# Performance work log

Measured on AMD Instinct MI355X. Metric: run time of the kernel, lower is better.

Reference implementation:

```python
import jax, jax.numpy as jnp
import numpy as np

# YOLOv2 anchors (grid units), 5 anchors, anchor_step=2
ANCHORS = np.array([[1.3221, 1.73145], [3.19275, 4.00944], [5.05587, 8.09892],
                    [9.47112, 4.84053], [11.2364, 10.0071]], dtype=np.float32)
NUM_CLASSES = 2
NOOBJECT_SCALE = 1.0
OBJECT_SCALE = 5.0
COORD_SCALE = 1.0
CLASS_SCALE = 1.0
SIL_THRESH = 0.6
T = 50  # max targets per image


def iou_cwh(b1, b2):
    # boxes (..., 4) as (cx, cy, w, h); broadcasting IoU, faithful to bbox_iou(x1y1x2y2=False)
    x1, y1, w1, h1 = b1[..., 0], b1[..., 1], b1[..., 2], b1[..., 3]
    x2, y2, w2, h2 = b2[..., 0], b2[..., 1], b2[..., 2], b2[..., 3]
    uw = jnp.maximum(x1 + w1 * 0.5, x2 + w2 * 0.5) - jnp.minimum(x1 - w1 * 0.5, x2 - w2 * 0.5)
    uh = jnp.maximum(y1 + h1 * 0.5, y2 + h2 * 0.5) - jnp.minimum(y1 - h1 * 0.5, y2 - h2 * 0.5)
    cw = w1 + w2 - uw
    ch = h1 + h2 - uh
    carea = jnp.where((cw <= 0) | (ch <= 0), 0.0, cw * ch)
    return carea / (w1 * h1 + w2 * h2 - carea)


def yolo_v2_loss(output, target):
    anchors = jnp.asarray(ANCHORS)
    nA, nC = anchors.shape[0], NUM_CLASSES
    nB, _, nH, nW = output.shape
    out5 = output.reshape(nB, nA, 5 + nC + 1, nH, nW)
    aw, ah = anchors[:, 0], anchors[:, 1]

    # ---------- detached predicted boxes (torch used .data) ----------
    po = jax.lax.stop_gradient(out5)
    gx_grid = jnp.arange(nW, dtype=output.dtype)
    gy_grid = jnp.arange(nH, dtype=output.dtype)
    px = jax.nn.sigmoid(po[:, :, 0]) + gx_grid[None, None, None, :]
    py = jax.nn.sigmoid(po[:, :, 1]) + gy_grid[None, None, :, None]
    pw = jnp.exp(po[:, :, 2]) * aw[None, :, None, None]
    ph = jnp.exp(po[:, :, 3]) * ah[None, :, None, None]
    pred = jnp.stack([px, py, pw, ph], -1).reshape(nB, nA * nH * nW, 4)  # (nB, nP, 4)

    # ---------- parse targets ----------
    tgt = target.reshape(nB, T, 6)  # (cls, x, y, w, h, lr)
    tcls_v = tgt[..., 0]
    gx = tgt[..., 1] * nW
    gy = tgt[..., 2] * nH
    gw = tgt[..., 3] * nW
    gh = tgt[..., 4] * nH
    lr_v = tgt[..., 5]
    # torch breaks at first x==0; emulate with cumulative validity
    valid = jnp.cumprod((tgt[..., 1] != 0).astype(jnp.int32), axis=1).astype(bool)

    # ---------- silence mask: max IoU of every pred box vs all gt ----------
    gt = jnp.stack([gx, gy, gw, gh], -1)  # (nB, T, 4)
    ious = iou_cwh(pred[:, :, None, :], gt[:, None, :, :])  # (nB, nP, T)
    cur_ious = jnp.where(valid[:, None, :], ious, 0.0).max(-1)  # (nB, nP)
    conf_mask0 = jnp.where(cur_ious > SIL_THRESH, 0.0, NOOBJECT_SCALE).reshape(-1)

    # ---------- best anchor per gt (centered IoU, argmax == first strict max) ----------
    z = jnp.zeros_like(gw)
    gt0 = jnp.stack([z, z, gw, gh], -1)[:, :, None, :]  # (nB, T, 1, 4)
    za = jnp.zeros_like(aw)
    an0 = jnp.stack([za, za, aw, ah], -1)[None, None, :, :]  # (1, 1, nA, 4)
    best_n = jnp.argmax(iou_cwh(an0, gt0), axis=-1)  # (nB, T)

    gi = gx.astype(jnp.int32)
    gj = gy.astype(jnp.int32)
    aw_b = aw[best_n]
    ah_b = ah[best_n]
    tx_v = gx - gi
    ty_v = gy - gj
    tw_v = jnp.log(gw / aw_b)
    th_v = jnp.log(gh / ah_b)
    idx_in_b = best_n * (nH * nW) + gj * nW + gi  # (nB, T)
    pred_at = jnp.take_along_axis(pred, idx_in_b[:, :, None], axis=1)  # (nB, T, 4)
    tconf_v = iou_cwh(gt, pred_at)  # (nB, T)

    Ntot = nB * nA * nH * nW
    flat_idx = jnp.where(valid, jnp.arange(nB)[:, None] * (nA * nH * nW) + idx_in_b, Ntot)
    one = jnp.ones_like(tx_v)
    # rows: coord_mask, cls_mask, conf_mask, tx, ty, tw, th, tconf, tcls, lr_mask, tconf_lr
    vals = jnp.stack([one, one, OBJECT_SCALE * one, tx_v, ty_v, tw_v, th_v,
                      tconf_v, tcls_v, one, lr_v], 0)  # (11, nB, T)
    state0 = jnp.zeros((11, Ntot), output.dtype).at[2].set(conf_mask0)

    def body(st, inp):
        i, v = inp
        return st.at[:, i].set(v, mode='drop'), None

    state, _ = jax.lax.scan(body, state0, (flat_idx.T, jnp.transpose(vals, (2, 0, 1))))
    state = jax.lax.stop_gradient(state)
    shp = (nB, nA, nH, nW)
    (coord_mask, cls_mask, conf_mask, tx, ty, tw, th,
     tconf, tcls, lr_mask, tconf_lr) = [state[i].reshape(shp) for i in range(11)]

    # ---------- differentiable predictions ----------
    x = jax.nn.sigmoid(out5[:, :, 0])
    y = jax.nn.sigmoid(out5[:, :, 1])
    w = out5[:, :, 2]
    h = out5[:, :, 3]
    conf = jax.nn.sigmoid(out5[:, :, 4])
    conf_lr = jax.nn.sigmoid(out5[:, :, 5 + nC])
    # torch: view(nB*nA, nC, nH*nW).transpose(1,2) -> row order (b, a, h, w)
    cls_logits = jnp.transpose(out5[:, :, 5:5 + nC], (0, 1, 3, 4, 2)).reshape(-1, nC)

    def mse_half(a, b, m):
        return 0.5 * jnp.sum((a * m - b * m) ** 2)

    loss_x = COORD_SCALE * mse_half(x, tx, coord_mask)
    loss_y = COORD_SCALE * mse_half(y, ty, coord_mask)
    loss_w = COORD_SCALE * mse_half(w, tw, coord_mask)
    loss_h = COORD_SCALE * mse_half(h, th, coord_mask)
    loss_conf = mse_half(conf, tconf, jnp.sqrt(conf_mask))
    logp = jax.nn.log_softmax(cls_logits, axis=-1)
    tcls_flat = tcls.reshape(-1).astype(jnp.int32)
    ce = -jnp.take_along_axis(logp, tcls_flat[:, None], axis=1)[:, 0]
    loss_cls = CLASS_SCALE * jnp.sum(ce * cls_mask.reshape(-1))
    loss_conf_lr = mse_half(conf_lr, tconf_lr, lr_mask)
    loss = loss_x + loss_y + loss_w + loss_h + loss_conf + loss_cls + 0.5 * loss_conf_lr
    return loss / nB


def setup_inputs() -> dict:
    key = jax.random.key(0)
    k1, k2, k3, k4, k5 = jax.random.split(key, 5)
    nB, nH, nW = 16, 96, 96
    nA, nC = 5, 2
    output = jax.random.normal(k1, (nB, nA * (5 + nC + 1), nH, nW), jnp.float32) * 0.5
    # targets: (cls, x, y, w, h, lr) per slot, all 50 slots valid (x != 0)
    cls = jax.random.randint(k2, (nB, T, 1), 0, nC).astype(jnp.float32)
    xy = jax.random.uniform(k3, (nB, T, 2), minval=0.05, maxval=0.95)
    wh = jax.random.uniform(k4, (nB, T, 2), minval=0.05, maxval=0.5)
    lr = jax.random.uniform(k5, (nB, T, 1))
    target = jnp.concatenate([cls, xy, wh, lr], axis=-1).reshape(nB, T * 6)
    return {"output": output, "target": target}


def reference(output, target):
    return yolo_v2_loss(output, target)
```

## Files before the change

kernel.cpp:

```cpp
#include <hip/hip_runtime.h>
#include <math.h>

#define NB 16
#define NA 5
#define NH 96
#define NW 96
#define TT 50
#define HW (NH*NW)
#define APB (NA*HW)
#define CPT 4

__device__ __constant__ float c_aw[NA] = {1.3221f, 3.19275f, 5.05587f, 9.47112f, 11.2364f};
__device__ __constant__ float c_ah[NA] = {1.73145f, 4.00944f, 8.09892f, 4.84053f, 10.0071f};

__device__ __forceinline__ float sigmoidf(float x) { return 1.0f / (1.0f + __expf(-x)); }

__global__ void prep_kernel(const float* __restrict__ target,
                            const float* __restrict__ outp,
                            float* __restrict__ gt,
                            float* __restrict__ out) {
    int b = blockIdx.x;
    int t = threadIdx.x;
    __shared__ float s_gxl[TT], s_gxr[TT], s_gyl[TT], s_gyr[TT], s_g06n[TT];
    __shared__ int   s_cell[TT], s_valid[TT];

    float xraw = (t < TT) ? target[(b*TT + t)*6 + 1] : 1.0f;
    unsigned long long m = __ballot(xraw != 0.0f);

    int valid = 0, best = 0, cell = -1, gi = 0, gj = 0;
    float gx=0, gy=0, gw=1, gh=1, tcls=0, lr=0;
    float gxl=0, gxr=0, gyl=0, gyr=0, g06n=-1e30f;
    if (t < TT) {
        valid = (((~m) & ((2ull << t) - 1ull)) == 0ull) ? 1 : 0;
        const float* tg = target + (b*TT + t)*6;
        tcls = tg[0];
        gx = tg[1]*NW; gy = tg[2]*NH; gw = tg[3]*NW; gh = tg[4]*NH;
        lr = tg[5];
        float bestiou = -1.0f;
        for (int a = 0; a < NA; ++a) {
            float inter = fminf(gw, c_aw[a]) * fminf(gh, c_ah[a]);
            float iou = inter / (gw*gh + c_aw[a]*c_ah[a] - inter);
            if (iou > bestiou) { bestiou = iou; best = a; }
        }
        gi = (int)gx; gj = (int)gy;
        cell = best*HW + gj*NW + gi;
        if (valid) {
            gxl = gx - 0.5f*gw; gxr = gx + 0.5f*gw;
            gyl = gy - 0.5f*gh; gyr = gy + 0.5f*gh;
            g06n = -0.6f*gw*gh;
        }
        s_gxl[t] = gxl; s_gxr[t] = gxr; s_gyl[t] = gyl; s_gyr[t] = gyr;
        s_g06n[t] = g06n;
        s_cell[t] = valid ? cell : -1;
        s_valid[t] = valid;
        float* r = gt + (b*TT + t)*8;
        r[0] = gxl; r[1] = gxr; r[2] = gyl; r[3] = gyr; r[4] = g06n;
        r[5] = 0.0f; r[6] = 0.0f; r[7] = 0.0f;
    }
    __syncthreads();

    float acc = 0.0f;
    if (t < TT && valid) {
        int winner = 1;
        for (int u = t + 1; u < TT; ++u)
            if (s_valid[u] && s_cell[u] == cell) { winner = 0; break; }
        if (winner) {
            int a = cell / HW;
            int rem = cell - a*HW;
            const float* base = outp + (size_t)((b*NA + a)*8)*HW + rem;
            float o0 = base[0*HW], o1 = base[1*HW], o2 = base[2*HW], o3 = base[3*HW];
            float o4 = base[4*HW], o5 = base[5*HW], o6 = base[6*HW], o7 = base[7*HW];
            float sx = sigmoidf(o0), sy = sigmoidf(o1);
            float px = sx + (float)gi, py = sy + (float)gj;
            float pw = __expf(o2) * c_aw[a];
            float ph = __expf(o3) * c_ah[a];
            float pxl = px - 0.5f*pw, pxr = px + 0.5f*pw;
            float pyl = py - 0.5f*ph, pyr = py + 0.5f*ph;
            float parea = pw*ph, p6 = 0.6f*parea;
            float maxv = -1e30f;
            for (int u = 0; u < TT; ++u) {
                float cw = fminf(pxr, s_gxr[u]) - fmaxf(pxl, s_gxl[u]);
                float ch = fminf(pyr, s_gyr[u]) - fmaxf(pyl, s_gyl[u]);
                float carea = fmaxf(cw, 0.0f) * fmaxf(ch, 0.0f);
                maxv = fmaxf(maxv, fmaf(1.6f, carea, s_g06n[u]));
            }
            float conf = sigmoidf(o4);
            float noobj = (maxv > p6) ? 0.0f : 0.5f*conf*conf;
            float cw = fminf(pxr, gxr) - fmaxf(pxl, gxl);
            float ch = fminf(pyr, gyr) - fmaxf(pyl, gyl);
            float carea = fmaxf(cw, 0.0f) * fmaxf(ch, 0.0f);
            float tconf = carea / (parea + gw*gh - carea);
            float dc = conf - tconf;
            acc = 2.5f*dc*dc;
            float tx = gx - (float)gi, ty = gy - (float)gj;
            float tw = logf(gw / c_aw[best]), th = logf(gh / c_ah[best]);
            float dx = sx - tx, dy = sy - ty, dw = o2 - tw, dh = o3 - th;
            acc += 0.5f*(dx*dx + dy*dy + dw*dw + dh*dh);
            float mm  = fmaxf(o5, o6);
            float lse = mm + __logf(__expf(o5 - mm) + __expf(o6 - mm));
            acc += lse - ((tcls != 0.0f) ? o6 : o5);
            float dl = sigmoidf(o7) - lr;
            acc += 0.25f*dl*dl;
            acc -= noobj;
        }
    }
    for (int off = 32; off > 0; off >>= 1) acc += __shfl_down(acc, off, 64);
    if (t == 0) atomicAdd(out, acc * (1.0f/NB));
}

__global__ __launch_bounds__(256)
void loss_kernel(const float* __restrict__ outp,
                 const float* __restrict__ gt,
                 float* __restrict__ loss) {
    int b   = blockIdx.y;
    int tid = threadIdx.x;
    int q     = blockIdx.x*256 + tid;
    int cell0 = q*CPT;
    int a   = cell0 / HW;
    int rem = cell0 - a*HW;
    int j   = rem / NW;
    int i0  = rem - j*NW;

    const float* base = outp + (size_t)((b*NA + a)*8)*HW + rem;
    float4 v0 = *(const float4*)(base + 0*HW);
    float4 v1 = *(const float4*)(base + 1*HW);
    float4 v2 = *(const float4*)(base + 2*HW);
    float4 v3 = *(const float4*)(base + 3*HW);
    float4 v4 = *(const float4*)(base + 4*HW);
    float o0[CPT] = {v0.x, v0.y, v0.z, v0.w};
    float o1[CPT] = {v1.x, v1.y, v1.z, v1.w};
    float o2[CPT] = {v2.x, v2.y, v2.z, v2.w};
    float o3[CPT] = {v3.x, v3.y, v3.z, v3.w};
    float o4[CPT] = {v4.x, v4.y, v4.z, v4.w};

    float aw = c_aw[a], ah = c_ah[a];
    float pxl[CPT], pxr[CPT], pyl[CPT], pyr[CPT], p6[CPT], maxv[CPT];
    #pragma unroll
    for (int c = 0; c < CPT; ++c) {
        float sx = sigmoidf(o0[c]), sy = sigmoidf(o1[c]);
        float px = sx + (float)(i0 + c);
        float py = sy + (float)j;
        float pw = __expf(o2[c]) * aw;
        float ph = __expf(o3[c]) * ah;
        pxl[c] = px - 0.5f*pw; pxr[c] = px + 0.5f*pw;
        pyl[c] = py - 0.5f*ph; pyr[c] = py + 0.5f*ph;
        p6[c]  = 0.6f*(pw*ph);
        maxv[c] = -1e30f;
    }

    const float* g = gt + b*(TT*8);
    #pragma unroll 2
    for (int t = 0; t < TT; ++t) {
        const float* r = g + t*8;
        float gxl = r[0], gxr = r[1], gyl = r[2], gyr = r[3], g06n = r[4];
        #pragma unroll
        for (int c = 0; c < CPT; ++c) {
            float cw = fminf(pxr[c], gxr) - fmaxf(pxl[c], gxl);
            float ch = fminf(pyr[c], gyr) - fmaxf(pyl[c], gyl);
            float carea = fmaxf(cw, 0.0f) * fmaxf(ch, 0.0f);
            maxv[c] = fmaxf(maxv[c], fmaf(1.6f, carea, g06n));
        }
    }

    float acc = 0.0f;
    #pragma unroll
    for (int c = 0; c < CPT; ++c) {
        float conf = sigmoidf(o4[c]);
        acc += (maxv[c] > p6[c]) ? 0.0f : 0.5f*conf*conf;
    }

    for (int off = 32; off > 0; off >>= 1) acc += __shfl_down(acc, off, 64);
    __shared__ float ssum[4];
    int lane = tid & 63, wid = tid >> 6;
    if (lane == 0) ssum[wid] = acc;
    __syncthreads();
    if (tid == 0) {
        float s = (ssum[0] + ssum[1]) + (ssum[2] + ssum[3]);
        atomicAdd(loss, s * (1.0f/NB));
    }
}

extern "C" void kernel_launch(void* const* d_in, const int* in_sizes, int n_in,
                              void* d_out, int out_size, void* d_ws, size_t ws_size,
                              hipStream_t stream) {
    const float* output = (const float*)d_in[0];
    const float* target = (const float*)d_in[1];
    float* gtbuf = (float*)d_ws;
    float* out   = (float*)d_out;

    hipMemsetAsync(out, 0, (size_t)out_size*sizeof(float), stream);
    hipLaunchKernelGGL(prep_kernel, dim3(NB), dim3(64), 0, stream,
                       target, output, gtbuf, out);
    dim3 grid(APB/(256*CPT), NB);
    hipLaunchKernelGGL(loss_kernel, grid, dim3(256), 0, stream,
                       output, gtbuf, out);
}
```

Measured before the change: 97.88 us.

## Move per-target object loss into main loss kernel via cell-to-target map

The prep kernel no longer computes object-cell losses. It writes ground-truth box data, per-target coefficients and a dense cell-to-target index map, which is cleared with a memset of 0xFF. The main kernel loads the box table into shared memory and, for each cell, either computes the full object loss or the no-object term. This removes the serial per-target work and the per-target global box re-reads. It adds a 2.9MB memset and an int4 map read per thread.

```diff
diff --git a/kernel.cpp b/kernel.cpp
--- a/kernel.cpp
+++ b/kernel.cpp
@@ -16,20 +16,18 @@
 __device__ __forceinline__ float sigmoidf(float x) { return 1.0f / (1.0f + __expf(-x)); }
 
 __global__ void prep_kernel(const float* __restrict__ target,
-                            const float* __restrict__ outp,
-                            float* __restrict__ gt,
-                            float* __restrict__ out) {
+                            float* __restrict__ gth,
+                            float* __restrict__ gtc,
+                            int* __restrict__ map) {
     int b = blockIdx.x;
     int t = threadIdx.x;
-    __shared__ float s_gxl[TT], s_gxr[TT], s_gyl[TT], s_gyr[TT], s_g06n[TT];
-    __shared__ int   s_cell[TT], s_valid[TT];
+    __shared__ int s_cell[TT], s_valid[TT];
 
     float xraw = (t < TT) ? target[(b*TT + t)*6 + 1] : 1.0f;
     unsigned long long m = __ballot(xraw != 0.0f);
 
     int valid = 0, best = 0, cell = -1, gi = 0, gj = 0;
     float gx=0, gy=0, gw=1, gh=1, tcls=0, lr=0;
-    float gxl=0, gxr=0, gyl=0, gyr=0, g06n=-1e30f;
     if (t < TT) {
         valid = (((~m) & ((2ull << t) - 1ull)) == 0ull) ? 1 : 0;
         const float* tg = target + (b*TT + t)*6;
@@ -44,76 +42,48 @@
         }
         gi = (int)gx; gj = (int)gy;
         cell = best*HW + gj*NW + gi;
-        if (valid) {
-            gxl = gx - 0.5f*gw; gxr = gx + 0.5f*gw;
-            gyl = gy - 0.5f*gh; gyr = gy + 0.5f*gh;
-            g06n = -0.6f*gw*gh;
-        }
-        s_gxl[t] = gxl; s_gxr[t] = gxr; s_gyl[t] = gyl; s_gyr[t] = gyr;
-        s_g06n[t] = g06n;
-        s_cell[t] = valid ? cell : -1;
+        s_cell[t]  = valid ? cell : -1;
         s_valid[t] = valid;
-        float* r = gt + (b*TT + t)*8;
-        r[0] = gxl; r[1] = gxr; r[2] = gyl; r[3] = gyr; r[4] = g06n;
-        r[5] = 0.0f; r[6] = 0.0f; r[7] = 0.0f;
     }
     __syncthreads();
-
-    float acc = 0.0f;
-    if (t < TT && valid) {
-        int winner = 1;
-        for (int u = t + 1; u < TT; ++u)
-            if (s_valid[u] && s_cell[u] == cell) { winner = 0; break; }
-        if (winner) {
-            int a = cell / HW;
-            int rem = cell - a*HW;
-            const float* base = outp + (size_t)((b*NA + a)*8)*HW + rem;
-            float o0 = base[0*HW], o1 = base[1*HW], o2 = base[2*HW], o3 = base[3*HW];
-            float o4 = base[4*HW], o5 = base[5*HW], o6 = base[6*HW], o7 = base[7*HW];
-            float sx = sigmoidf(o0), sy = sigmoidf(o1);
-            float px = sx + (float)gi, py = sy + (float)gj;
-            float pw = __expf(o2) * c_aw[a];
-            float ph = __expf(o3) * c_ah[a];
-            float pxl = px - 0.5f*pw, pxr = px + 0.5f*pw;
-            float pyl = py - 0.5f*ph, pyr = py + 0.5f*ph;
-            float parea = pw*ph, p6 = 0.6f*parea;
-            float maxv = -1e30f;
-            for (int u = 0; u < TT; ++u) {
-                float cw = fminf(pxr, s_gxr[u]) - fmaxf(pxl, s_gxl[u]);
-                float ch = fminf(pyr, s_gyr[u]) - fmaxf(pyl, s_gyl[u]);
-                float carea = fmaxf(cw, 0.0f) * fmaxf(ch, 0.0f);
-                maxv = fmaxf(maxv, fmaf(1.6f, carea, s_g06n[u]));
-            }
-            float conf = sigmoidf(o4);
-            float noobj = (maxv > p6) ? 0.0f : 0.5f*conf*conf;
-            float cw = fminf(pxr, gxr) - fmaxf(pxl, gxl);
-            float ch = fminf(pyr, gyr) - fmaxf(pyl, gyl);
-            float carea = fmaxf(cw, 0.0f) * fmaxf(ch, 0.0f);
-            float tconf = carea / (parea + gw*gh - carea);
-            float dc = conf - tconf;
-            acc = 2.5f*dc*dc;
-            float tx = gx - (float)gi, ty = gy - (float)gj;
-            float tw = logf(gw / c_aw[best]), th = logf(gh / c_ah[best]);
-            float dx = sx - tx, dy = sy - ty, dw = o2 - tw, dh = o3 - th;
-            acc += 0.5f*(dx*dx + dy*dy + dw*dw + dh*dh);
-            float mm  = fmaxf(o5, o6);
-            float lse = mm + __logf(__expf(o5 - mm) + __expf(o6 - mm));
-            acc += lse - ((tcls != 0.0f) ? o6 : o5);
-            float dl = sigmoidf(o7) - lr;
-            acc += 0.25f*dl*dl;
-            acc -= noobj;
+    if (t < TT) {
+        float* rh = gth + (b*TT + t)*8;
+        if (valid) {
+            rh[0] = gx - 0.5f*gw; rh[1] = gx + 0.5f*gw;
+            rh[2] = gy - 0.5f*gh; rh[3] = gy + 0.5f*gh;
+            rh[4] = -0.6f*gw*gh;
+        } else {
+            rh[0] = 0.0f; rh[1] = 0.0f; rh[2] = 0.0f; rh[3] = 0.0f;
+            rh[4] = -1e30f;
+        }
+        rh[5] = 0.0f; rh[6] = 0.0f; rh[7] = 0.0f;
+        float* rc = gtc + (b*TT + t)*8;
+        rc[0] = gw*gh;
+        rc[1] = gx - (float)gi;  rc[2] = gy - (float)gj;
+        rc[3] = logf(gw / c_aw[best]); rc[4] = logf(gh / c_ah[best]);
+        rc[5] = tcls; rc[6] = lr; rc[7] = 0.0f;
+        if (valid) {
+            int winner = 1;
+            for (int u = t + 1; u < TT; ++u)
+                if (s_valid[u] && s_cell[u] == cell) { winner = 0; break; }
+            if (winner) map[b*APB + cell] = t;
         }
     }
-    for (int off = 32; off > 0; off >>= 1) acc += __shfl_down(acc, off, 64);
-    if (t == 0) atomicAdd(out, acc * (1.0f/NB));
 }
 
 __global__ __launch_bounds__(256)
 void loss_kernel(const float* __restrict__ outp,
-                 const float* __restrict__ gt,
+                 const float* __restrict__ gth,
+                 const float* __restrict__ gtc,
+                 const int* __restrict__ map,
                  float* __restrict__ loss) {
+    __shared__ float4 sgt4[TT*2];
+    float* sgt = (float*)sgt4;
     int b   = blockIdx.y;
     int tid = threadIdx.x;
+    if (tid < TT*2) sgt4[tid] = ((const float4*)(gth + b*TT*8))[tid];
+    __syncthreads();
+
     int q     = blockIdx.x*256 + tid;
     int cell0 = q*CPT;
     int a   = cell0 / HW;
@@ -134,7 +104,7 @@
     float o4[CPT] = {v4.x, v4.y, v4.z, v4.w};
 
     float aw = c_aw[a], ah = c_ah[a];
-    float pxl[CPT], pxr[CPT], pyl[CPT], pyr[CPT], p6[CPT], maxv[CPT];
+    float pxl[CPT], pxr[CPT], pyl[CPT], pyr[CPT], parea[CPT], maxv[CPT];
     #pragma unroll
     for (int c = 0; c < CPT; ++c) {
         float sx = sigmoidf(o0[c]), sy = sigmoidf(o1[c]);
@@ -144,29 +114,56 @@
         float ph = __expf(o3[c]) * ah;
         pxl[c] = px - 0.5f*pw; pxr[c] = px + 0.5f*pw;
         pyl[c] = py - 0.5f*ph; pyr[c] = py + 0.5f*ph;
-        p6[c]  = 0.6f*(pw*ph);
+        parea[c] = pw*ph;
         maxv[c] = -1e30f;
     }
 
-    const float* g = gt + b*(TT*8);
-    #pragma unroll 2
+    #pragma unroll 10
     for (int t = 0; t < TT; ++t) {
-        const float* r = g + t*8;
-        float gxl = r[0], gxr = r[1], gyl = r[2], gyr = r[3], g06n = r[4];
+        float4 ra  = *(const float4*)(sgt + t*8);
+        float g06n = sgt[t*8 + 4];
         #pragma unroll
         for (int c = 0; c < CPT; ++c) {
-            float cw = fminf(pxr[c], gxr) - fmaxf(pxl[c], gxl);
-            float ch = fminf(pyr[c], gyr) - fmaxf(pyl[c], gyl);
+            float cw = fminf(pxr[c], ra.y) - fmaxf(pxl[c], ra.x);
+            float ch = fminf(pyr[c], ra.w) - fmaxf(pyl[c], ra.z);
             float carea = fmaxf(cw, 0.0f) * fmaxf(ch, 0.0f);
             maxv[c] = fmaxf(maxv[c], fmaf(1.6f, carea, g06n));
         }
     }
 
+    int4 mp = *(const int4*)(map + b*APB + cell0);
+    int mc[CPT] = {mp.x, mp.y, mp.z, mp.w};
+
     float acc = 0.0f;
     #pragma unroll
     for (int c = 0; c < CPT; ++c) {
         float conf = sigmoidf(o4[c]);
-        acc += (maxv[c] > p6[c]) ? 0.0f : 0.5f*conf*conf;
+        int tw_idx = mc[c];
+        if (tw_idx >= 0) {
+            const float* cr = gtc + (b*TT + tw_idx)*8;
+            float garea = cr[0], tx = cr[1], ty = cr[2];
+            float tw = cr[3], th = cr[4], tcls = cr[5], lr = cr[6];
+            float gxl = sgt[tw_idx*8+0], gxr = sgt[tw_idx*8+1];
+            float gyl = sgt[tw_idx*8+2], gyr = sgt[tw_idx*8+3];
+            float cw = fminf(pxr[c], gxr) - fmaxf(pxl[c], gxl);
+            float ch = fminf(pyr[c], gyr) - fmaxf(pyl[c], gyl);
+            float carea = fmaxf(cw, 0.0f) * fmaxf(ch, 0.0f);
+            float tconf = carea / (parea[c] + garea - carea);
+            float dc = conf - tconf;
+            float term = 2.5f*dc*dc;
+            float sx = sigmoidf(o0[c]), sy = sigmoidf(o1[c]);
+            float dx = sx - tx, dy = sy - ty, dw = o2[c] - tw, dh = o3[c] - th;
+            term += 0.5f*(dx*dx + dy*dy + dw*dw + dh*dh);
+            float o5 = base[5*HW + c], o6 = base[6*HW + c], o7 = base[7*HW + c];
+            float mm  = fmaxf(o5, o6);
+            float lse = mm + __logf(__expf(o5 - mm) + __expf(o6 - mm));
+            term += lse - ((tcls != 0.0f) ? o6 : o5);
+            float dl = sigmoidf(o7) - lr;
+            term += 0.25f*dl*dl;
+            acc += term;
+        } else {
+            acc += (maxv[c] > 0.6f*parea[c]) ? 0.0f : 0.5f*conf*conf;
+        }
     }
 
     for (int off = 32; off > 0; off >>= 1) acc += __shfl_down(acc, off, 64);
@@ -185,13 +182,16 @@
                               hipStream_t stream) {
     const float* output = (const float*)d_in[0];
     const float* target = (const float*)d_in[1];
-    float* gtbuf = (float*)d_ws;
-    float* out   = (float*)d_out;
+    float* gth = (float*)d_ws;
+    float* gtc = gth + NB*TT*8;
+    int*   map = (int*)((char*)d_ws + 65536);
+    float* out = (float*)d_out;
 
     hipMemsetAsync(out, 0, (size_t)out_size*sizeof(float), stream);
+    hipMemsetAsync(map, 0xFF, (size_t)NB*APB*sizeof(int), stream);
     hipLaunchKernelGGL(prep_kernel, dim3(NB), dim3(64), 0, stream,
-                       target, output, gtbuf, out);
+                       target, gth, gtc, map);
     dim3 grid(APB/(256*CPT), NB);
     hipLaunchKernelGGL(loss_kernel, grid, dim3(256), 0, stream,
-                       output, gtbuf, out);
+                       output, gth, gtc, map, out);
 }
```

Result: faster. 94.92 us (-3.0%).
